# Kernel tuning notes

Measured on AMD Instinct MI355X. Metric: run time of the kernel, lower is better.

The kernel has to match this reference:

```python
import jax, jax.numpy as jnp
from jax import lax
import numpy as np

B, T, D = 1024, 64, 512   # batch, obs_len, input_size
HD = 512                  # hidden_size
L = 3                     # n_layers
FN = 64                   # num_filters
OH = 1                    # output_horizon
ATTN_LEN = T - 1          # conv kernel height
FEAT = HD                 # feat_size = attn_size - filter_size + 1, filter_size=1


def setup_inputs() -> dict:
    key = jax.random.key(0)
    ks = jax.random.split(key, 12)
    s = 0.02
    x = jax.random.normal(ks[0], (B, T, D), dtype=jnp.float32)
    # stacked LSTM weights (input_size == hidden_size so layer-0 stacks cleanly)
    W_ih = jax.random.normal(ks[1], (L, 4 * HD, HD), dtype=jnp.float32) * s
    W_hh = jax.random.normal(ks[2], (L, 4 * HD, HD), dtype=jnp.float32) * s
    b_ih = jax.random.normal(ks[3], (L, 4 * HD), dtype=jnp.float32) * s
    b_hh = jax.random.normal(ks[4], (L, 4 * HD), dtype=jnp.float32) * s
    # TPA: Conv2d(1, FN, (ATTN_LEN, 1)) in torch layout [FN, 1, ATTN_LEN, 1]
    conv_W = jax.random.normal(ks[5], (FN, 1, ATTN_LEN, 1), dtype=jnp.float32) * s
    conv_b = jax.random.normal(ks[6], (FN,), dtype=jnp.float32) * s
    lin1_W = jax.random.normal(ks[7], (FN, HD), dtype=jnp.float32) * s
    lin1_b = jax.random.normal(ks[8], (FN,), dtype=jnp.float32) * s
    lin2_W = jax.random.normal(ks[9], (HD, HD + FN), dtype=jnp.float32) * s
    lin2_b = jnp.zeros((HD,), dtype=jnp.float32)
    out_W = jax.random.normal(ks[10], (OH, HD), dtype=jnp.float32) * s
    out_b = jnp.zeros((OH,), dtype=jnp.float32)
    return dict(x=x, W_ih=W_ih, W_hh=W_hh, b_ih=b_ih, b_hh=b_hh,
                conv_W=conv_W, conv_b=conv_b, lin1_W=lin1_W, lin1_b=lin1_b,
                lin2_W=lin2_W, lin2_b=lin2_b, out_W=out_W, out_b=out_b)


def _lstm_last_layer_hs(x, W_ih, W_hh, b_ih, b_hh):
    """Run L-layer LSTM over time, return last-layer hidden per step [T,B,HD]."""
    h0 = jnp.zeros((L, B, HD), x.dtype)
    c0 = jnp.zeros((L, B, HD), x.dtype)

    def step(carry, xt):
        h, c = carry  # [L,B,HD]
        inp = xt
        hs, cs = [], []
        for l in range(L):  # small fixed layer count
            gates = inp @ W_ih[l].T + h[l] @ W_hh[l].T + b_ih[l] + b_hh[l]
            i, f, g, o = jnp.split(gates, 4, axis=-1)  # torch gate order i,f,g,o
            cl = jax.nn.sigmoid(f) * c[l] + jax.nn.sigmoid(i) * jnp.tanh(g)
            hl = jax.nn.sigmoid(o) * jnp.tanh(cl)
            hs.append(hl)
            cs.append(cl)
            inp = hl
        return (jnp.stack(hs), jnp.stack(cs)), hs[-1]

    _, ys = lax.scan(step, (h0, c0), jnp.swapaxes(x, 0, 1))
    return ys  # [T,B,HD]


def reference(x, W_ih, W_hh, b_ih, b_hh, conv_W, conv_b,
              lin1_W, lin1_b, lin2_W, lin2_b, out_W, out_b):
    ys = _lstm_last_layer_hs(x, W_ih, W_hh, b_ih, b_hh)   # [T,B,HD]
    htt = ys[-1]                                          # [B,HD] final hidden
    H = jax.nn.relu(jnp.swapaxes(ys[:-1], 0, 1))          # [B,T-1,HD]

    # Conv2d(1,FN,(T-1,1)) over [B,1,T-1,HD]: contracts the time axis only
    kW = conv_W[:, 0, :, 0]                               # [FN,T-1]
    conv_bcf = jnp.einsum('btf,ct->bcf', H, kW) + conv_b[:, None]  # [B,FN,FEAT]
    # torch .view(-1, feat_size, filter_num) on contiguous [B,FN,1,FEAT]
    conv_vecs = jax.nn.relu(conv_bcf.reshape(B, FEAT, FN))         # [B,FEAT,FN]

    w = htt @ lin1_W.T + lin1_b                           # [B,FN]
    s = jnp.sum(conv_vecs * w[:, None, :], axis=2)        # [B,FEAT]
    alpha = jax.nn.sigmoid(s)
    v = jnp.sum(alpha[:, :, None] * conv_vecs, axis=1)    # [B,FN]

    concat = jnp.concatenate([htt, v], axis=1)            # [B,HD+FN]
    new_ht = concat @ lin2_W.T + lin2_b                   # [B,HD]
    ypred = (new_ht @ out_W.T + out_b)[:, :, None]        # [B,OH,1]
    return ypred
```

## Files before the change

### kernel.cpp

```cpp
#include <hip/hip_runtime.h>
#include <hip/hip_bf16.h>


typedef short v8s __attribute__((ext_vector_type(8)));
typedef float v4f __attribute__((ext_vector_type(4)));
typedef __hip_bfloat16 bf16;

#define B_   1024
#define T_   64
#define D_   512
#define HD_  512

__device__ __forceinline__ float sigm(float v) { return 1.0f / (1.0f + __expf(-v)); }
__device__ __forceinline__ float tanh_(float v) { return 2.0f / (1.0f + __expf(-2.0f * v)) - 1.0f; }
__device__ __forceinline__ float b2f(bf16 v) { return __bfloat162float(v); }
__device__ __forceinline__ float bu2f(ushort u) {
  union { unsigned i; float f; } x; x.i = ((unsigned)u) << 16; return x.f;
}

__device__ __forceinline__ void cvt_store8(ushort* dst, const float* src) {
  float4 a = *(const float4*)src;
  float4 b = *(const float4*)(src + 4);
  bf16 h[8] = {__float2bfloat16(a.x), __float2bfloat16(a.y),
               __float2bfloat16(a.z), __float2bfloat16(a.w),
               __float2bfloat16(b.x), __float2bfloat16(b.y),
               __float2bfloat16(b.z), __float2bfloat16(b.w)};
  *(uint4*)dst = *(const uint4*)h;
}

__device__ __forceinline__ void glds16(const bf16* g, ushort* l) {
  __builtin_amdgcn_global_load_lds(
      (const __attribute__((address_space(1))) void*)g,
      (__attribute__((address_space(3))) void*)l, 16, 0, 0);
}

constexpr size_t SZ_YS = (size_t)T_ * B_ * HD_ * 2;
constexpr size_t SZ_HB = (size_t)2 * 2 * B_ * HD_ * 2;
constexpr size_t SZ_CB = (size_t)3 * B_ * HD_ * 4;
constexpr size_t SZ_ZP = (size_t)B_ * HD_ * 2;
constexpr size_t SZ_WV = (size_t)B_ * 64 * 4;
constexpr size_t SZ_VB = (size_t)B_ * 64 * 4;
constexpr size_t SZ_WB = (size_t)3 * 2048 * 1024 * 2;
constexpr size_t SZ_KC = (size_t)64 * 64 * 2;
constexpr size_t SZ_FW = (size_t)640 * 4;
constexpr size_t SZ_XB = (size_t)T_ * B_ * D_ * 2;
constexpr size_t O_YS = 0;
constexpr size_t O_HB = O_YS + SZ_YS;
constexpr size_t O_CB = O_HB + SZ_HB;
constexpr size_t O_ZP = O_CB + SZ_CB;
constexpr size_t O_WV = O_ZP + SZ_ZP;
constexpr size_t O_VB = O_WV + SZ_WV;
constexpr size_t O_WB = O_VB + SZ_VB;
constexpr size_t O_KC = O_WB + SZ_WB;
constexpr size_t O_FW = O_KC + SZ_KC;
constexpr size_t O_XB = O_FW + SZ_FW;

__global__ __launch_bounds__(256) void prep_w(const float* __restrict__ Wih,
                                              const float* __restrict__ Whh,
                                              bf16* __restrict__ Wbuf) {
  int tf = blockIdx.x * 256 + threadIdx.x;
  int group = tf >> 10;
  int layer = group >> 8, rem = group & 255;
  int nt = rem >> 4, ch = rem & 15;
  int li = tf & 1023;
  int frag = li >> 6, lane = li & 63;
  int nb = frag >> 1, kk = frag & 1;
  int c = lane & 15, q = lane >> 4;
  int half = nb >> 2, gate = nb & 3;
  int j = nt * 32 + half * 16 + c;
  int R = gate * 512 + j;
  int k = (ch & 7) * 64 + kk * 32 + q * 8;
  const float* src = ((ch < 8) ? Wih : Whh) + ((size_t)layer * 2048 + R) * 512 + k;
  cvt_store8((ushort*)(Wbuf + (size_t)tf * 8), src);
}

__global__ __launch_bounds__(256) void prep_x(const float* __restrict__ x,
                                              bf16* __restrict__ xb) {
  int idx = blockIdx.x * 256 + threadIdx.x;
  int d8 = idx & 63;
  int bt = idx >> 6;
  int b = bt & 1023, t = bt >> 10;
  cvt_store8((ushort*)(xb + ((size_t)t * B_ + b) * D_ + d8 * 8),
             x + ((size_t)b * T_ + t) * D_ + d8 * 8);
}

__global__ __launch_bounds__(256) void prep_kc(const float* __restrict__ convW,
                                               bf16* __restrict__ kC) {
  int idx = blockIdx.x * 256 + threadIdx.x;
  int c = idx >> 6, t = idx & 63;
  kC[idx] = __float2bfloat16(t < 63 ? convW[c * 63 + t] : 0.f);
}

__global__ __launch_bounds__(64) void prep_fw(const float* __restrict__ lin2W,
                                              const float* __restrict__ lin2b,
                                              const float* __restrict__ outW,
                                              const float* __restrict__ outb,
                                              float* __restrict__ fw) {
  const int blk = blockIdx.x, tid = threadIdx.x;
  if (blk < 9) {
    const int k = blk * 64 + tid;
    float a = 0.f;
    for (int j = 0; j < 512; ++j) a += outW[j] * lin2W[(size_t)j * 576 + k];
    fw[k] = a;
  } else {
    float a = 0.f;
    for (int j = tid; j < 512; j += 64) a += outW[j] * lin2b[j];
    for (int m = 1; m < 64; m <<= 1) a += __shfl_xor(a, m);
    if (tid == 0) fw[576] = a + outb[0];
  }
}

__global__ __launch_bounds__(512, 6) void lstm_stage(
    const bf16* __restrict__ xb, const bf16* __restrict__ Wbuf,
    const float* __restrict__ bih, const float* __restrict__ bhh,
    bf16* __restrict__ ys, bf16* __restrict__ hbuf, float* __restrict__ cbuf,
    const bf16* __restrict__ zp, int s, int llo) {
  __shared__ ushort As[2][4096];
  __shared__ ushort Bs[2][8192];

  const int layer = llo + (blockIdx.x >> 8);
  const int tile = blockIdx.x & 255;
  const int t = s - layer;
  const int mt = tile >> 4, nt = tile & 15;
  const int b0 = mt << 6;
  const int p = s & 1;

  bf16* hw = (layer < 2) ? hbuf + ((size_t)p * 2 + layer) * (B_ * HD_)
                         : ys + (size_t)t * (B_ * HD_);
  const bf16* srcA0 = (layer == 0)
      ? xb + (size_t)t * (B_ * D_)
      : hbuf + ((size_t)(p ^ 1) * 2 + (layer - 1)) * (B_ * HD_);
  const bf16* srcA1 = (layer < 2)
      ? hbuf + ((size_t)(p ^ 1) * 2 + layer) * (B_ * HD_)
      : ((t == 0) ? zp : ys + (size_t)(t - 1) * (B_ * HD_));
  const bf16* Wb = Wbuf + ((size_t)layer * 16 + nt) * 16 * 8192;

  const int tid = threadIdx.x, lane = tid & 63, w = tid >> 6;
  const int c = lane & 15, q = lane >> 4;
  const int wm = w >> 1, wn = w & 1;

  v4f acc[4];
#pragma unroll
  for (int ni = 0; ni < 4; ++ni) acc[ni] = v4f{0.f, 0.f, 0.f, 0.f};

  auto STAGE = [&](int ch, int pb) {
    const int kof = (ch & 7) * 64;
    const bf16* wsrc = Wb + (size_t)ch * 8192;
    const bf16* sA = (ch < 8) ? srcA0 : srcA1;
#pragma unroll
    for (int i = 0; i < 3; ++i) {
      int idx = w * 3 + i;
      if (idx < 16) {
        glds16(wsrc + idx * 512 + lane * 8, &Bs[pb][idx * 512]);
      } else {
        int f = idx - 16, mb = f >> 1, k2 = f & 1;
        glds16(sA + (size_t)(b0 + mb * 16 + c) * HD_ + kof + k2 * 32 + q * 8,
               &As[pb][f * 512]);
      }
    }
  };

  STAGE(0, 0);
  __syncthreads();

  for (int ch = 0; ch < 16; ++ch) {
    const int pb = ch & 1;
    if (ch < 15) STAGE(ch + 1, pb ^ 1);
    __builtin_amdgcn_s_setprio(1);
#pragma unroll
    for (int kk = 0; kk < 2; ++kk) {
      v8s af = *(const v8s*)&As[pb][(wm * 2 + kk) * 512 + lane * 8];
#pragma unroll
      for (int ni = 0; ni < 4; ++ni) {
        v8s bfr = *(const v8s*)&Bs[pb][((wn * 4 + ni) * 2 + kk) * 512 + lane * 8];
        acc[ni] = __builtin_amdgcn_mfma_f32_16x16x32_bf16(af, bfr, acc[ni], 0, 0, 0);
      }
    }
    __builtin_amdgcn_s_setprio(0);
    __syncthreads();
  }

  float* cl = cbuf + (size_t)layer * (B_ * HD_);
  const size_t bb = (size_t)layer * 2048;
  const int j = nt * 32 + wn * 16 + c;
  float bsum[4];
#pragma unroll
  for (int g4 = 0; g4 < 4; ++g4)
    bsum[g4] = bih[bb + g4 * 512 + j] + bhh[bb + g4 * 512 + j];
#pragma unroll
  for (int r = 0; r < 4; ++r) {
    const int b = b0 + wm * 16 + q * 4 + r;
    float iv = acc[0][r] + bsum[0];
    float fv = acc[1][r] + bsum[1];
    float gv = acc[2][r] + bsum[2];
    float ov = acc[3][r] + bsum[3];
    size_t off = (size_t)b * HD_ + j;
    float cprev = cl[off];
    float cn = sigm(fv) * cprev + sigm(iv) * tanh_(gv);
    float hn = sigm(ov) * tanh_(cn);
    cl[off] = cn;
    hw[off] = __float2bfloat16(hn);
  }
}

__global__ __launch_bounds__(64) void k0_lin1(const bf16* __restrict__ ys,
                                              const float* __restrict__ lin1W,
                                              const float* __restrict__ lin1b,
                                              float* __restrict__ wv) {
  __shared__ float htt[HD_];
  const int b = blockIdx.x, tid = threadIdx.x;
  for (int i = tid; i < HD_; i += 64)
    htt[i] = b2f(ys[((size_t)(T_ - 1) * B_ + b) * HD_ + i]);
  __syncthreads();
  float a = lin1b[tid];
  const float* wr = lin1W + (size_t)tid * HD_;
  for (int k = 0; k < HD_; k += 4) {
    float4 w4 = *(const float4*)(wr + k);
    a += htt[k] * w4.x + htt[k + 1] * w4.y + htt[k + 2] * w4.z + htt[k + 3] * w4.w;
  }
  wv[(size_t)b * 64 + tid] = a;
}

__global__ __launch_bounds__(256) void k1_attn(const bf16* __restrict__ ys,
                                               const bf16* __restrict__ kCb,
                                               const float* __restrict__ convb,
                                               const float* __restrict__ wvg,
                                               float* __restrict__ vbuf) {
  __shared__ ushort Ht[32768];
  const int b = blockIdx.x;
  const int tid = threadIdx.x, lane = tid & 63, w = tid >> 6;
  const int l15 = lane & 15, q = lane >> 4;
  char* HtB = (char*)Ht;

  for (int idx = tid; idx < 2048; idx += 256) {
    int f8 = (idx & 7) | (((idx >> 6) & 7) << 3);
    int t2 = ((idx >> 3) & 7) | ((idx >> 9) << 3);
    int t = t2 * 2;
    v8s ha = *(const v8s*)(ys + ((size_t)t * B_ + b) * HD_ + f8 * 8);
    v8s hb;
    if (t2 == 31) {
      hb = v8s{0, 0, 0, 0, 0, 0, 0, 0};
    } else {
      hb = *(const v8s*)(ys + ((size_t)(t + 1) * B_ + b) * HD_ + f8 * 8);
    }
#pragma unroll
    for (int e = 0; e < 8; ++e) {
      ushort lo = (ha[e] & (short)0x8000) ? (ushort)0 : (ushort)ha[e];
      ushort hi = (hb[e] & (short)0x8000) ? (ushort)0 : (ushort)hb[e];
      int f = f8 * 8 + e;
      int chunk = ((t >> 3) ^ (f & 7) ^ ((f >> 3) & 7)) & 7;
      *(unsigned*)(HtB + f * 128 + chunk * 16 + (t & 7) * 2) =
          (unsigned)lo | ((unsigned)hi << 16);
    }
  }
  __syncthreads();

  v8s af[4][2];
#pragma unroll
  for (int mi = 0; mi < 4; ++mi)
#pragma unroll
    for (int kk = 0; kk < 2; ++kk)
      af[mi][kk] = *(const v8s*)(kCb + (mi * 16 + l15) * 64 + kk * 32 + q * 8);

  v4f acc[4][8];
#pragma unroll
  for (int mi = 0; mi < 4; ++mi)
#pragma unroll
    for (int ni = 0; ni < 8; ++ni) acc[mi][ni] = v4f{0.f, 0.f, 0.f, 0.f};

#pragma unroll
  for (int ni = 0; ni < 8; ++ni) {
    const int f = w * 128 + ni * 16 + l15;
#pragma unroll
    for (int kk = 0; kk < 2; ++kk) {
      const int t0 = kk * 32 + q * 8;
      const int chunk = ((t0 >> 3) ^ (f & 7) ^ ((f >> 3) & 7)) & 7;
      v8s bf = *(const v8s*)(HtB + f * 128 + chunk * 16);
#pragma unroll
      for (int mi = 0; mi < 4; ++mi)
        acc[mi][ni] = __builtin_amdgcn_mfma_f32_16x16x32_bf16(af[mi][kk], bf, acc[mi][ni], 0, 0, 0);
    }
  }

  float cb[4][4];
#pragma unroll
  for (int mi = 0; mi < 4; ++mi)
#pragma unroll
    for (int r = 0; r < 4; ++r) cb[mi][r] = convb[mi * 16 + q * 4 + r];
  float wl[4];
#pragma unroll
  for (int nl = 0; nl < 4; ++nl) wl[nl] = wvg[(size_t)b * 64 + nl * 16 + l15];

#pragma unroll
  for (int mi = 0; mi < 4; ++mi)
#pragma unroll
    for (int ni = 0; ni < 8; ++ni)
#pragma unroll
      for (int r = 0; r < 4; ++r)
        acc[mi][ni][r] = fmaxf(acc[mi][ni][r] + cb[mi][r], 0.f);

  float al[4][4][2];
#pragma unroll
  for (int mi = 0; mi < 4; ++mi)
#pragma unroll
    for (int r = 0; r < 4; ++r)
#pragma unroll
      for (int nh = 0; nh < 2; ++nh) {
        float s = 0.f;
#pragma unroll
        for (int nl = 0; nl < 4; ++nl)
          s += acc[mi][nh * 4 + nl][r] * wl[nl];
        s += __shfl_xor(s, 1); s += __shfl_xor(s, 2);
        s += __shfl_xor(s, 4); s += __shfl_xor(s, 8);
        al[mi][r][nh] = sigm(s);
      }

  float vp[4];
#pragma unroll
  for (int nl = 0; nl < 4; ++nl) {
    float v = 0.f;
#pragma unroll
    for (int mi = 0; mi < 4; ++mi)
#pragma unroll
      for (int r = 0; r < 4; ++r)
#pragma unroll
      for (int nh = 0; nh < 2; ++nh)
        v += al[mi][r][nh] * acc[mi][nh * 4 + nl][r];
    v += __shfl_xor(v, 16);
    v += __shfl_xor(v, 32);
    vp[nl] = v;
  }
  if (lane < 16) {
#pragma unroll
    for (int nl = 0; nl < 4; ++nl)
      atomicAdd(&vbuf[(size_t)b * 64 + nl * 16 + l15], vp[nl]);
  }
}

__global__ __launch_bounds__(64) void k3_out(const bf16* __restrict__ ys,
                                             const float* __restrict__ vbuf,
                                             const float* __restrict__ fw,
                                             float* __restrict__ out) {
  const int b = blockIdx.x, tid = threadIdx.x;
  v8s h = *(const v8s*)(ys + ((size_t)(T_ - 1) * B_ + b) * HD_ + tid * 8);
  const float4 w4a = *(const float4*)(fw + tid * 8);
  const float4 w4b = *(const float4*)(fw + tid * 8 + 4);
  float a = bu2f((ushort)h[0]) * w4a.x + bu2f((ushort)h[1]) * w4a.y +
            bu2f((ushort)h[2]) * w4a.z + bu2f((ushort)h[3]) * w4a.w +
            bu2f((ushort)h[4]) * w4b.x + bu2f((ushort)h[5]) * w4b.y +
            bu2f((ushort)h[6]) * w4b.z + bu2f((ushort)h[7]) * w4b.w;
  a += vbuf[(size_t)b * 64 + tid] * fw[512 + tid];
  for (int m = 1; m < 64; m <<= 1) a += __shfl_xor(a, m);
  if (tid == 0) out[b] = a + fw[576];
}

extern "C" void kernel_launch(void* const* d_in, const int* in_sizes, int n_in,
                              void* d_out, int out_size, void* d_ws, size_t ws_size,
                              hipStream_t stream) {
  const float* x     = (const float*)d_in[0];
  const float* Wih   = (const float*)d_in[1];
  const float* Whh   = (const float*)d_in[2];
  const float* bih   = (const float*)d_in[3];
  const float* bhh   = (const float*)d_in[4];
  const float* convW = (const float*)d_in[5];
  const float* convb = (const float*)d_in[6];
  const float* lin1W = (const float*)d_in[7];
  const float* lin1b = (const float*)d_in[8];
  const float* lin2W = (const float*)d_in[9];
  const float* lin2b = (const float*)d_in[10];
  const float* outW  = (const float*)d_in[11];
  const float* outb  = (const float*)d_in[12];

  char* ws = (char*)d_ws;
  bf16*  ys   = (bf16*)(ws + O_YS);
  bf16*  hbuf = (bf16*)(ws + O_HB);
  float* cbuf = (float*)(ws + O_CB);
  bf16*  zp   = (bf16*)(ws + O_ZP);
  float* wv   = (float*)(ws + O_WV);
  float* vbuf = (float*)(ws + O_VB);
  bf16*  Wbuf = (bf16*)(ws + O_WB);
  bf16*  kCb  = (bf16*)(ws + O_KC);
  float* fwv  = (float*)(ws + O_FW);
  bf16*  xb   = (bf16*)(ws + O_XB);

  hipMemsetAsync(hbuf, 0, SZ_HB, stream);
  hipMemsetAsync(cbuf, 0, SZ_CB, stream);
  hipMemsetAsync((void*)zp, 0, SZ_ZP, stream);
  hipMemsetAsync(vbuf, 0, SZ_VB, stream);

  prep_w<<<3072, 256, 0, stream>>>(Wih, Whh, Wbuf);
  prep_x<<<16384, 256, 0, stream>>>(x, xb);
  prep_kc<<<16, 256, 0, stream>>>(convW, kCb);
  prep_fw<<<10, 64, 0, stream>>>(lin2W, lin2b, outW, outb, fwv);

  for (int s = 0; s < T_ + 3 - 1; ++s) {
    int llo = (s > T_ - 1) ? (s - (T_ - 1)) : 0;
    int lhi = (s < 2) ? s : 2;
    int cnt = lhi - llo + 1;
    lstm_stage<<<cnt * 256, 512, 0, stream>>>(xb, Wbuf, bih, bhh, ys, hbuf,
                                              cbuf, zp, s, llo);
  }

  k0_lin1<<<B_, 64, 0, stream>>>(ys, lin1W, lin1b, wv);
  k1_attn<<<B_, 256, 0, stream>>>(ys, kCb, convb, wv, vbuf);
  k3_out<<<B_, 64, 0, stream>>>(ys, vbuf, fwv, (float*)d_out);
}
```

Before: 1.985 ms.

## Replace per-step LSTM launches with persistent kernel and global atomic barrier

Turns the 66 wavefront-step kernel launches into one persistent kernel of 512 blocks that loops over steps, grid-strides through each step's tiles, and synchronises steps with an atomic-counter spin barrier in global memory. The aim is to remove per-launch overhead and the tail/drain gaps between dependent launches. It relies on all 512 blocks being co-resident (occupancy hint lowered to 4 per SIMD-group), otherwise the barrier deadlocks. Cross-block visibility of the h/c writes also depends on the acquire/release atomics. Blocks that have no tile in a step still spin, and the first- and last-step imbalance remains.

After: 6.529 ms. 3.29x slower.

```diff
diff --git a/kernel.cpp b/kernel.cpp
--- a/kernel.cpp
+++ b/kernel.cpp
@@ -44,6 +44,7 @@
 constexpr size_t SZ_KC = (size_t)64 * 64 * 2;
 constexpr size_t SZ_FW = (size_t)640 * 4;
 constexpr size_t SZ_XB = (size_t)T_ * B_ * D_ * 2;
+constexpr size_t SZ_BC = (size_t)64;
 constexpr size_t O_YS = 0;
 constexpr size_t O_HB = O_YS + SZ_YS;
 constexpr size_t O_CB = O_HB + SZ_HB;
@@ -54,6 +55,7 @@
 constexpr size_t O_KC = O_WB + SZ_WB;
 constexpr size_t O_FW = O_KC + SZ_KC;
 constexpr size_t O_XB = O_FW + SZ_FW;
+constexpr size_t O_BC = O_XB + SZ_XB;
 
 __global__ __launch_bounds__(256) void prep_w(const float* __restrict__ Wih,
                                               const float* __restrict__ Whh,
@@ -110,96 +112,114 @@
   }
 }
 
-__global__ __launch_bounds__(512, 6) void lstm_stage(
+__global__ __launch_bounds__(512, 4) void lstm_pers(
     const bf16* __restrict__ xb, const bf16* __restrict__ Wbuf,
     const float* __restrict__ bih, const float* __restrict__ bhh,
     bf16* __restrict__ ys, bf16* __restrict__ hbuf, float* __restrict__ cbuf,
-    const bf16* __restrict__ zp, int s, int llo) {
+    const bf16* __restrict__ zp, int* __restrict__ bar) {
   __shared__ ushort As[2][4096];
   __shared__ ushort Bs[2][8192];
 
-  const int layer = llo + (blockIdx.x >> 8);
-  const int tile = blockIdx.x & 255;
-  const int t = s - layer;
-  const int mt = tile >> 4, nt = tile & 15;
-  const int b0 = mt << 6;
-  const int p = s & 1;
-
-  bf16* hw = (layer < 2) ? hbuf + ((size_t)p * 2 + layer) * (B_ * HD_)
-                         : ys + (size_t)t * (B_ * HD_);
-  const bf16* srcA0 = (layer == 0)
-      ? xb + (size_t)t * (B_ * D_)
-      : hbuf + ((size_t)(p ^ 1) * 2 + (layer - 1)) * (B_ * HD_);
-  const bf16* srcA1 = (layer < 2)
-      ? hbuf + ((size_t)(p ^ 1) * 2 + layer) * (B_ * HD_)
-      : ((t == 0) ? zp : ys + (size_t)(t - 1) * (B_ * HD_));
-  const bf16* Wb = Wbuf + ((size_t)layer * 16 + nt) * 16 * 8192;
-
+  const int bid = blockIdx.x;
   const int tid = threadIdx.x, lane = tid & 63, w = tid >> 6;
   const int c = lane & 15, q = lane >> 4;
   const int wm = w >> 1, wn = w & 1;
 
-  v4f acc[4];
-#pragma unroll
-  for (int ni = 0; ni < 4; ++ni) acc[ni] = v4f{0.f, 0.f, 0.f, 0.f};
-
-  auto STAGE = [&](int ch, int pb) {
-    const int kof = (ch & 7) * 64;
-    const bf16* wsrc = Wb + (size_t)ch * 8192;
-    const bf16* sA = (ch < 8) ? srcA0 : srcA1;
-#pragma unroll
-    for (int i = 0; i < 3; ++i) {
-      int idx = w * 3 + i;
-      if (idx < 16) {
-        glds16(wsrc + idx * 512 + lane * 8, &Bs[pb][idx * 512]);
-      } else {
-        int f = idx - 16, mb = f >> 1, k2 = f & 1;
-        glds16(sA + (size_t)(b0 + mb * 16 + c) * HD_ + kof + k2 * 32 + q * 8,
-               &As[pb][f * 512]);
+  for (int s = 0; s < T_ + 2; ++s) {
+    const int llo = (s > T_ - 1) ? (s - (T_ - 1)) : 0;
+    const int lhi = (s < 2) ? s : 2;
+    const int njobs = (lhi - llo + 1) * 256;
+    const int p = s & 1;
+
+    for (int jg = bid; jg < njobs; jg += 512) {
+      const int layer = llo + (jg >> 8);
+      const int tile = jg & 255;
+      const int t = s - layer;
+      const int mt = tile >> 4, nt = tile & 15;
+      const int b0 = mt << 6;
+
+      bf16* hw = (layer < 2) ? hbuf + ((size_t)p * 2 + layer) * (B_ * HD_)
+                             : ys + (size_t)t * (B_ * HD_);
+      const bf16* srcA0 = (layer == 0)
+          ? xb + (size_t)t * (B_ * D_)
+          : hbuf + ((size_t)(p ^ 1) * 2 + (layer - 1)) * (B_ * HD_);
+      const bf16* srcA1 = (layer < 2)
+          ? ((t == 0) ? zp : hbuf + ((size_t)(p ^ 1) * 2 + layer) * (B_ * HD_))
+          : ((t == 0) ? zp : ys + (size_t)(t - 1) * (B_ * HD_));
+      const bf16* Wb = Wbuf + ((size_t)layer * 16 + nt) * 16 * 8192;
+
+      v4f acc[4];
+#pragma unroll
+      for (int ni = 0; ni < 4; ++ni) acc[ni] = v4f{0.f, 0.f, 0.f, 0.f};
+
+      auto STAGE = [&](int ch, int pb) {
+        const int kof = (ch & 7) * 64;
+        const bf16* wsrc = Wb + (size_t)ch * 8192;
+        const bf16* sA = (ch < 8) ? srcA0 : srcA1;
+#pragma unroll
+        for (int i = 0; i < 3; ++i) {
+          int idx = w * 3 + i;
+          if (idx < 16) {
+            glds16(wsrc + idx * 512 + lane * 8, &Bs[pb][idx * 512]);
+          } else {
+            int f = idx - 16, mb = f >> 1, k2 = f & 1;
+            glds16(sA + (size_t)(b0 + mb * 16 + c) * HD_ + kof + k2 * 32 + q * 8,
+                   &As[pb][f * 512]);
+          }
+        }
+      };
+
+      STAGE(0, 0);
+      __syncthreads();
+
+      for (int ch = 0; ch < 16; ++ch) {
+        const int pb = ch & 1;
+        if (ch < 15) STAGE(ch + 1, pb ^ 1);
+        __builtin_amdgcn_s_setprio(1);
+#pragma unroll
+        for (int kk = 0; kk < 2; ++kk) {
+          v8s af = *(const v8s*)&As[pb][(wm * 2 + kk) * 512 + lane * 8];
+#pragma unroll
+          for (int ni = 0; ni < 4; ++ni) {
+            v8s bfr = *(const v8s*)&Bs[pb][((wn * 4 + ni) * 2 + kk) * 512 + lane * 8];
+            acc[ni] = __builtin_amdgcn_mfma_f32_16x16x32_bf16(af, bfr, acc[ni], 0, 0, 0);
+          }
+        }
+        __builtin_amdgcn_s_setprio(0);
+        __syncthreads();
+      }
+
+      float* cl = cbuf + (size_t)layer * (B_ * HD_);
+      const size_t bb = (size_t)layer * 2048;
+      const int j = nt * 32 + wn * 16 + c;
+      float bsum[4];
+#pragma unroll
+      for (int g4 = 0; g4 < 4; ++g4)
+        bsum[g4] = bih[bb + g4 * 512 + j] + bhh[bb + g4 * 512 + j];
+#pragma unroll
+      for (int r = 0; r < 4; ++r) {
+        const int b = b0 + wm * 16 + q * 4 + r;
+        float iv = acc[0][r] + bsum[0];
+        float fv = acc[1][r] + bsum[1];
+        float gv = acc[2][r] + bsum[2];
+        float ov = acc[3][r] + bsum[3];
+        size_t off = (size_t)b * HD_ + j;
+        float cprev = cl[off];
+        float cn = sigm(fv) * cprev + sigm(iv) * tanh_(gv);
+        float hn = sigm(ov) * tanh_(cn);
+        cl[off] = cn;
+        hw[off] = __float2bfloat16(hn);
       }
     }
-  };
-
-  STAGE(0, 0);
-  __syncthreads();
-
-  for (int ch = 0; ch < 16; ++ch) {
-    const int pb = ch & 1;
-    if (ch < 15) STAGE(ch + 1, pb ^ 1);
-    __builtin_amdgcn_s_setprio(1);
-#pragma unroll
-    for (int kk = 0; kk < 2; ++kk) {
-      v8s af = *(const v8s*)&As[pb][(wm * 2 + kk) * 512 + lane * 8];
-#pragma unroll
-      for (int ni = 0; ni < 4; ++ni) {
-        v8s bfr = *(const v8s*)&Bs[pb][((wn * 4 + ni) * 2 + kk) * 512 + lane * 8];
-        acc[ni] = __builtin_amdgcn_mfma_f32_16x16x32_bf16(af, bfr, acc[ni], 0, 0, 0);
-      }
+
+    __syncthreads();
+    if (tid == 0) {
+      __hip_atomic_fetch_add(bar, 1, __ATOMIC_ACQ_REL, __HIP_MEMORY_SCOPE_AGENT);
+      const int target = 512 * (s + 1);
+      while (__hip_atomic_load(bar, __ATOMIC_ACQUIRE, __HIP_MEMORY_SCOPE_AGENT) < target)
+        __builtin_amdgcn_s_sleep(16);
     }
-    __builtin_amdgcn_s_setprio(0);
     __syncthreads();
-  }
-
-  float* cl = cbuf + (size_t)layer * (B_ * HD_);
-  const size_t bb = (size_t)layer * 2048;
-  const int j = nt * 32 + wn * 16 + c;
-  float bsum[4];
-#pragma unroll
-  for (int g4 = 0; g4 < 4; ++g4)
-    bsum[g4] = bih[bb + g4 * 512 + j] + bhh[bb + g4 * 512 + j];
-#pragma unroll
-  for (int r = 0; r < 4; ++r) {
-    const int b = b0 + wm * 16 + q * 4 + r;
-    float iv = acc[0][r] + bsum[0];
-    float fv = acc[1][r] + bsum[1];
-    float gv = acc[2][r] + bsum[2];
-    float ov = acc[3][r] + bsum[3];
-    size_t off = (size_t)b * HD_ + j;
-    float cprev = cl[off];
-    float cn = sigm(fv) * cprev + sigm(iv) * tanh_(gv);
-    float hn = sigm(ov) * tanh_(cn);
-    cl[off] = cn;
-    hw[off] = __float2bfloat16(hn);
   }
 }
 
@@ -382,24 +402,21 @@
   bf16*  kCb  = (bf16*)(ws + O_KC);
   float* fwv  = (float*)(ws + O_FW);
   bf16*  xb   = (bf16*)(ws + O_XB);
+  int*   bar  = (int*)(ws + O_BC);
 
   hipMemsetAsync(hbuf, 0, SZ_HB, stream);
   hipMemsetAsync(cbuf, 0, SZ_CB, stream);
   hipMemsetAsync((void*)zp, 0, SZ_ZP, stream);
   hipMemsetAsync(vbuf, 0, SZ_VB, stream);
+  hipMemsetAsync(bar, 0, SZ_BC, stream);
 
   prep_w<<<3072, 256, 0, stream>>>(Wih, Whh, Wbuf);
   prep_x<<<16384, 256, 0, stream>>>(x, xb);
   prep_kc<<<16, 256, 0, stream>>>(convW, kCb);
   prep_fw<<<10, 64, 0, stream>>>(lin2W, lin2b, outW, outb, fwv);
 
-  for (int s = 0; s < T_ + 3 - 1; ++s) {
-    int llo = (s > T_ - 1) ? (s - (T_ - 1)) : 0;
-    int lhi = (s < 2) ? s : 2;
-    int cnt = lhi - llo + 1;
-    lstm_stage<<<cnt * 256, 512, 0, stream>>>(xb, Wbuf, bih, bhh, ys, hbuf,
-                                              cbuf, zp, s, llo);
-  }
+  lstm_pers<<<512, 512, 0, stream>>>(xb, Wbuf, bih, bhh, ys, hbuf, cbuf, zp,
+                                     bar);
 
   k0_lin1<<<B_, 64, 0, stream>>>(ys, lin1W, lin1b, wv);
   k1_attn<<<B_, 256, 0, stream>>>(ys, kCb, convb, wv, vbuf);
```
